# Kernel tuning notes

Measured on AMD Instinct MI355X. Metric: run time of the kernel, lower is better.

The kernel has to match this reference:

```python
import jax, jax.numpy as jnp
import numpy as np

B, N, DIM = 4, 4096, 1024
HEADS, DFF, WIN = 16, 4096, 128
EPS = 1e-5


def _layernorm(x, w, b):
    mu = jnp.mean(x, axis=-1, keepdims=True)
    var = jnp.mean(jnp.square(x - mu), axis=-1, keepdims=True)
    return (x - mu) * jax.lax.rsqrt(var + EPS) * w + b


def _local_attention(q, k, v, window):
    # q,k,v: (B, h, N, d); non-causal, look_backward=1, look_forward=1
    Bq, h, n, d = q.shape
    nb = n // window
    scale = d ** -0.5
    q = q.reshape(Bq * h, nb, window, d) * scale
    k = k.reshape(Bq * h, nb, window, d)
    v = v.reshape(Bq * h, nb, window, d)

    def look_around(t):  # (BH, nb, w, d) -> (BH, nb, 3w, d)
        tp = jnp.pad(t, ((0, 0), (1, 1), (0, 0), (0, 0)))
        return jnp.concatenate([tp[:, :-2], tp[:, 1:-1], tp[:, 2:]], axis=2)

    kk = look_around(k)
    vv = look_around(v)

    # validity mask for out-of-range look-around buckets
    idx = jnp.arange(n).reshape(nb, window)
    idx_p = jnp.pad(idx, ((1, 1), (0, 0)), constant_values=-1)
    kidx = jnp.concatenate([idx_p[:-2], idx_p[1:-1], idx_p[2:]], axis=1)  # (nb, 3w)
    valid = (kidx >= 0)[None, :, None, :]  # (1, nb, 1, 3w)

    sim = jnp.einsum('bnid,bnjd->bnij', q, kk)  # (BH, nb, w, 3w)
    neg = jnp.finfo(sim.dtype).min
    sim = jnp.where(valid, sim, neg)
    attn = jax.nn.softmax(sim, axis=-1)
    out = jnp.einsum('bnij,bnjd->bnid', attn, vv)
    return out.reshape(Bq, h, n, d)


def setup_inputs() -> dict:
    key = jax.random.key(0)
    ks = jax.random.split(key, 8)
    w = lambda k, shape: jax.random.normal(k, shape, jnp.float32) * 0.02
    return {
        'x': jax.random.normal(ks[0], (B, N, DIM), jnp.float32),
        'ln1_w': jnp.ones((DIM,), jnp.float32), 'ln1_b': jnp.zeros((DIM,), jnp.float32),
        'qkv_w': w(ks[1], (3 * DIM, DIM)), 'qkv_b': jnp.zeros((3 * DIM,), jnp.float32),
        'proj_w': w(ks[2], (DIM, DIM)), 'proj_b': jnp.zeros((DIM,), jnp.float32),
        'ln2_w': jnp.ones((DIM,), jnp.float32), 'ln2_b': jnp.zeros((DIM,), jnp.float32),
        'fc1_w': w(ks[3], (DFF, DIM)), 'fc1_b': jnp.zeros((DFF,), jnp.float32),
        'fc2_w': w(ks[4], (DIM, DFF)), 'fc2_b': jnp.zeros((DIM,), jnp.float32),
    }


def reference(x, ln1_w, ln1_b, qkv_w, qkv_b, proj_w, proj_b, ln2_w, ln2_b, fc1_w, fc1_b, fc2_w, fc2_b):
    Bx, n, C = x.shape
    h = HEADS
    hd = C // h
    x_norm = _layernorm(x, ln1_w, ln1_b)
    qkv = x_norm @ qkv_w.T + qkv_b  # (B, N, 3C)
    qkv = qkv.reshape(Bx, n, 3, h, hd).transpose(2, 0, 3, 1, 4)  # (3, B, h, N, hd)
    q, k, v = qkv[0], qkv[1], qkv[2]
    attn_out = _local_attention(q, k, v, WIN)  # (B, h, N, hd)
    attn_out = attn_out.transpose(0, 2, 1, 3).reshape(Bx, n, C)
    x = x + (attn_out @ proj_w.T + proj_b)
    y = _layernorm(x, ln2_w, ln2_b)
    y = jax.nn.gelu(y @ fc1_w.T + fc1_b, approximate=False)
    x = x + (y @ fc2_w.T + fc2_b)
    return x
```

## Files before the change

### kernel.cpp

```cpp
#include <hip/hip_runtime.h>
#include <math.h>

typedef unsigned short u16;
typedef __attribute__((ext_vector_type(4))) float f32x4;
typedef __attribute__((ext_vector_type(8))) __bf16 bf16x8;
typedef __attribute__((ext_vector_type(8))) u16 u16x8;
typedef __attribute__((ext_vector_type(4))) u16 u16x4;

__device__ __forceinline__ float bf2f(u16 v) {
    unsigned int u = ((unsigned int)v) << 16;
    return __builtin_bit_cast(float, u);
}
__device__ __forceinline__ u16 f2bf(float f) {
    unsigned int x = __builtin_bit_cast(unsigned int, f);
    x += 0x7fffu + ((x >> 16) & 1u);
    return (u16)(x >> 16);
}

__device__ __forceinline__ void load_lds16(const u16* g, u16* l) {
    __builtin_amdgcn_global_load_lds((const __attribute__((address_space(1))) void*)g,
                                     (__attribute__((address_space(3))) void*)l, 16, 0, 0);
}

#define WAIT_VM(N) asm volatile("s_waitcnt vmcnt(" #N ")" ::: "memory")
#define LGKM0_SB() do { asm volatile("s_waitcnt lgkmcnt(0)" ::: "memory"); \
                        __builtin_amdgcn_sched_barrier(0); } while (0)
#define MFMA16(d, x, y) d = __builtin_amdgcn_mfma_f32_16x16x32_bf16(x, y, d, 0, 0, 0)

__global__ __launch_bounds__(256) void cvt_kernel(const float* __restrict__ in,
                                                  u16* __restrict__ out, int n)
{
    const int i = (blockIdx.x * 256 + threadIdx.x) * 4;
    if (i >= n) return;
    const float4 f = *(const float4*)(in + i);
    u16x4 o;
    o[0] = f2bf(f.x); o[1] = f2bf(f.y); o[2] = f2bf(f.z); o[3] = f2bf(f.w);
    *(u16x4*)(out + i) = o;
}

template<int EPI, int RES, bool OF32, int NFR>
__global__ __launch_bounds__(512, 2) void gemm256(
    const u16* __restrict__ A, const u16* __restrict__ W,
    const float* __restrict__ bias,
    const float* __restrict__ resf, const u16* __restrict__ resb,
    void* __restrict__ O0v, u16* __restrict__ O1, u16* __restrict__ O2,
    int M, int N, int K, int lda, int ldw, int mbase)
{
    constexpr int BBASE = 16384;
    constexpr int BUFU  = 16384 + NFR * 4096;
    __shared__ u16 S[2 * BUFU];
    const int tid  = threadIdx.x;
    const int w    = tid >> 6;
    const int l    = tid & 63;
    const int colq = l & 15;
    const int quad = l >> 4;
    const int w3   = w & 3;
    const int wm   = (w >> 2) * 128;
    const int wn   = w3 * (NFR * 16);

    const int nX  = (int)gridDim.x;
    const int nwg = nX * (int)gridDim.y;
    const int did = (int)blockIdx.y * nX + (int)blockIdx.x;
    const int q8  = nwg >> 3;
    const int wg  = (nwg & 7) ? did : ((did & 7) * q8 + (did >> 3));
    const int bm  = wg / nX;
    const int bn  = wg - bm * nX;
    const int m0  = bm * 256, n0 = bn * (NFR * 64);

    const int rw   = l >> 3;
    const int sseg = ((l & 7) ^ rw) * 8;
    const u16* gA[2][2];
    const u16* gB[2][2];
#pragma unroll
    for (int h = 0; h < 2; ++h)
#pragma unroll
        for (int j = 0; j < 2; ++j) {
            const int rr = w * 16 + j * 8 + rw;
            gA[h][j] = A + (size_t)(m0 + h * 128 + rr) * lda + sseg;
            if constexpr (NFR == 4) {
                const int nl = (rr >> 5) * 64 + (h * 2 + ((rr >> 4) & 1)) * 16 + (rr & 15);
                gB[h][j] = W + (size_t)(n0 + nl) * ldw + sseg;
            } else if (h == 0) {
                gB[0][j] = W + (size_t)(n0 + rr) * ldw + sseg;
            }
        }
    const int lw = w * 1024;

    const int c0 = (quad * 8) ^ ((colq & 7) << 3);
    const int c1 = c0 ^ 32;

    f32x4 acc[8][NFR] = {};

#pragma unroll
    for (int h = 0; h < 2; ++h)
#pragma unroll
        for (int j = 0; j < 2; ++j)
            load_lds16(gA[h][j], S + h * 8192 + lw + j * 512);
    load_lds16(gB[0][0], S + BBASE + lw);
    load_lds16(gB[0][1], S + BBASE + lw + 512);
    if constexpr (NFR == 4) {
        load_lds16(gB[1][0], S + BBASE + 8192 + lw);
        load_lds16(gB[1][1], S + BBASE + 8192 + lw + 512);
        WAIT_VM(2);
    } else {
        WAIT_VM(0);
    }
    __builtin_amdgcn_s_barrier();

    const int NT = K >> 6;
    for (int t = 0; t < NT; ++t) {
        u16* Sc = S + (t & 1) * BUFU;
        u16* Sn = S + ((t + 1) & 1) * BUFU;
        const int  kk = (t + 1) << 6;
        const bool pf = (t + 1) < NT;

        if constexpr (NFR == 4) {
            bf16x8 aL[4][2], aH[4][2], bL[2][2], bH[2][2];

#pragma unroll
            for (int m = 0; m < 4; ++m) {
                const int rb = (wm + m * 16 + colq) * 64;
                aL[m][0] = *(const bf16x8*)(Sc + rb + c0);
                aL[m][1] = *(const bf16x8*)(Sc + rb + c1);
            }
#pragma unroll
            for (int n = 0; n < 2; ++n) {
                const int rb = BBASE + (w3 * 32 + n * 16 + colq) * 64;
                bL[n][0] = *(const bf16x8*)(Sc + rb + c0);
                bL[n][1] = *(const bf16x8*)(Sc + rb + c1);
            }
            if (pf) {
#pragma unroll
                for (int h = 0; h < 2; ++h)
#pragma unroll
                    for (int j = 0; j < 2; ++j)
                        load_lds16(gA[h][j] + kk, Sn + h * 8192 + lw + j * 512);
            }
            __builtin_amdgcn_s_barrier();
            LGKM0_SB();
            __builtin_amdgcn_s_setprio(1);
#pragma unroll
            for (int m = 0; m < 4; ++m)
#pragma unroll
                for (int n = 0; n < 2; ++n) {
                    MFMA16(acc[m][n], aL[m][0], bL[n][0]);
                    MFMA16(acc[m][n], aL[m][1], bL[n][1]);
                }
            __builtin_amdgcn_s_setprio(0);
            if (pf) { WAIT_VM(4); } else { WAIT_VM(0); }
            __builtin_amdgcn_s_barrier();

#pragma unroll
            for (int n = 0; n < 2; ++n) {
                const int rb = BBASE + 8192 + (w3 * 32 + n * 16 + colq) * 64;
                bH[n][0] = *(const bf16x8*)(Sc + rb + c0);
                bH[n][1] = *(const bf16x8*)(Sc + rb + c1);
            }
            if (pf) {
                load_lds16(gB[0][0] + kk, Sn + BBASE + lw);
                load_lds16(gB[0][1] + kk, Sn + BBASE + lw + 512);
            }
            __builtin_amdgcn_s_barrier();
            LGKM0_SB();
            __builtin_amdgcn_s_setprio(1);
#pragma unroll
            for (int m = 0; m < 4; ++m)
#pragma unroll
                for (int n = 0; n < 2; ++n) {
                    MFMA16(acc[m][2 + n], aL[m][0], bH[n][0]);
                    MFMA16(acc[m][2 + n], aL[m][1], bH[n][1]);
                }
            __builtin_amdgcn_s_setprio(0);
            __builtin_amdgcn_s_barrier();

#pragma unroll
            for (int m = 0; m < 4; ++m) {
                const int rb = (wm + 64 + m * 16 + colq) * 64;
                aH[m][0] = *(const bf16x8*)(Sc + rb + c0);
                aH[m][1] = *(const bf16x8*)(Sc + rb + c1);
            }
            if (pf) {
                load_lds16(gB[1][0] + kk, Sn + BBASE + 8192 + lw);
                load_lds16(gB[1][1] + kk, Sn + BBASE + 8192 + lw + 512);
            }
            __builtin_amdgcn_s_barrier();
            LGKM0_SB();
            __builtin_amdgcn_s_setprio(1);
#pragma unroll
            for (int m = 0; m < 4; ++m)
#pragma unroll
                for (int n = 0; n < 2; ++n) {
                    MFMA16(acc[4 + m][n], aH[m][0], bL[n][0]);
                    MFMA16(acc[4 + m][n], aH[m][1], bL[n][1]);
                }
            __builtin_amdgcn_s_setprio(0);
            __builtin_amdgcn_s_barrier();

            __builtin_amdgcn_s_setprio(1);
#pragma unroll
            for (int m = 0; m < 4; ++m)
#pragma unroll
                for (int n = 0; n < 2; ++n) {
                    MFMA16(acc[4 + m][2 + n], aH[m][0], bH[n][0]);
                    MFMA16(acc[4 + m][2 + n], aH[m][1], bH[n][1]);
                }
            __builtin_amdgcn_s_setprio(0);
            if (pf) { WAIT_VM(2); }
            __builtin_amdgcn_s_barrier();
        } else {
            bf16x8 aL[4][2], aH[4][2], bb[2][2];

#pragma unroll
            for (int m = 0; m < 4; ++m) {
                const int rb = (wm + m * 16 + colq) * 64;
                aL[m][0] = *(const bf16x8*)(Sc + rb + c0);
                aL[m][1] = *(const bf16x8*)(Sc + rb + c1);
            }
#pragma unroll
            for (int n = 0; n < 2; ++n) {
                const int rb = BBASE + (w3 * 32 + n * 16 + colq) * 64;
                bb[n][0] = *(const bf16x8*)(Sc + rb + c0);
                bb[n][1] = *(const bf16x8*)(Sc + rb + c1);
            }
            if (pf) {
#pragma unroll
                for (int h = 0; h < 2; ++h)
#pragma unroll
                    for (int j = 0; j < 2; ++j)
                        load_lds16(gA[h][j] + kk, Sn + h * 8192 + lw + j * 512);
            }
            __builtin_amdgcn_s_barrier();
            LGKM0_SB();
            __builtin_amdgcn_s_setprio(1);
#pragma unroll
            for (int m = 0; m < 4; ++m)
#pragma unroll
                for (int n = 0; n < 2; ++n) {
                    MFMA16(acc[m][n], aL[m][0], bb[n][0]);
                    MFMA16(acc[m][n], aL[m][1], bb[n][1]);
                }
            __builtin_amdgcn_s_setprio(0);
            __builtin_amdgcn_s_barrier();

#pragma unroll
            for (int m = 0; m < 4; ++m) {
                const int rb = (wm + 64 + m * 16 + colq) * 64;
                aH[m][0] = *(const bf16x8*)(Sc + rb + c0);
                aH[m][1] = *(const bf16x8*)(Sc + rb + c1);
            }
            if (pf) {
                load_lds16(gB[0][0] + kk, Sn + BBASE + lw);
                load_lds16(gB[0][1] + kk, Sn + BBASE + lw + 512);
            }
            __builtin_amdgcn_s_barrier();
            LGKM0_SB();
            __builtin_amdgcn_s_setprio(1);
#pragma unroll
            for (int m = 0; m < 4; ++m)
#pragma unroll
                for (int n = 0; n < 2; ++n) {
                    MFMA16(acc[4 + m][n], aH[m][0], bb[n][0]);
                    MFMA16(acc[4 + m][n], aH[m][1], bb[n][1]);
                }
            __builtin_amdgcn_s_setprio(0);
            WAIT_VM(0);
            __builtin_amdgcn_s_barrier();
        }
    }

    if constexpr (EPI == 0) {
        if (n0 >= 2048) {
            __syncthreads();
#pragma unroll
            for (int nf = 0; nf < NFR; ++nf) {
                const int cl = wn + nf * 16 + colq;
                const float bz = bias[n0 + cl];
                const int swz = (cl & 7) << 3;
#pragma unroll
                for (int mf = 0; mf < 8; ++mf) {
                    const int rb = wm + mf * 16 + quad * 4;
                    u16x4 pk;
#pragma unroll
                    for (int i = 0; i < 4; ++i) pk[i] = f2bf(acc[mf][nf][i] + bz);
                    *(u16x4*)(S + cl * 256 + (rb ^ swz)) = pk;
                }
            }
            __syncthreads();
            const int cl   = tid >> 1;
            const int c    = n0 + cl;
            const int head = (c >> 6) & 15;
            const int d    = c & 63;
            const int rg0  = mbase + m0;
            const int bh   = (rg0 >> 12) * 16 + head;
            const int half = tid & 1;
            const int swz  = (cl & 7) << 3;
            u16* op = O2 + ((size_t)bh * 64 + d) * 4096 + (rg0 & 4095) + half * 128;
#pragma unroll
            for (int j = 0; j < 16; ++j) {
                const int r0 = half * 128 + j * 8;
                *(u16x8*)(op + j * 8) = *(const u16x8*)(S + cl * 256 + (r0 ^ swz));
            }
            return;
        }
    }
#pragma unroll
    for (int nf = 0; nf < NFR; ++nf) {
        const int c = n0 + wn + nf * 16 + colq;
        const float bz = bias ? bias[c] : 0.f;
#pragma unroll
        for (int mf = 0; mf < 8; ++mf) {
#pragma unroll
            for (int i = 0; i < 4; ++i) {
                const int r = m0 + wm + mf * 16 + quad * 4 + i;
                float v = acc[mf][nf][i] + bz;
                if constexpr (EPI == 0) {
                    const int head = (c >> 6) & 15;
                    const int d    = c & 63;
                    const int rg   = mbase + r;
                    const int tt   = rg & 4095;
                    const int bh   = (rg >> 12) * 16 + head;
                    const u16 val = f2bf(v);
                    if (c < 1024) ((u16*)O0v)[((size_t)bh * 4096 + tt) * 64 + d] = val;
                    else          O1[((size_t)bh * 4096 + tt) * 64 + d] = val;
                } else {
                    const size_t idx = (size_t)r * N + c;
                    if constexpr (RES == 1) v += resf[idx];
                    if constexpr (RES == 2) v += bf2f(resb[idx]);
                    if constexpr (EPI == 2) v = 0.5f * v * (1.0f + erff(v * 0.70710678118654752f));
                    if constexpr (OF32) ((float*)O0v)[idx] = v;
                    else                ((u16*)O0v)[idx] = f2bf(v);
                }
            }
        }
    }
}

template<bool F32IN>
__global__ __launch_bounds__(256) void ln_kernel(
    const void* __restrict__ xin, const float* __restrict__ w,
    const float* __restrict__ b, u16* __restrict__ out)
{
    const int wave = threadIdx.x >> 6, lane = threadIdx.x & 63;
    const size_t row = (size_t)blockIdx.x * 4 + wave;
    float v[16];
    if constexpr (F32IN) {
        const float* xr = (const float*)xin + row * 1024 + lane * 16;
#pragma unroll
        for (int j = 0; j < 4; ++j) {
            const float4 f = *(const float4*)(xr + j * 4);
            v[j * 4 + 0] = f.x; v[j * 4 + 1] = f.y; v[j * 4 + 2] = f.z; v[j * 4 + 3] = f.w;
        }
    } else {
        const u16* xr = (const u16*)xin + row * 1024 + lane * 16;
        u16x8 xa = *(const u16x8*)xr;
        u16x8 xb = *(const u16x8*)(xr + 8);
#pragma unroll
        for (int i = 0; i < 8; ++i) { v[i] = bf2f(xa[i]); v[8 + i] = bf2f(xb[i]); }
    }
    float s = 0.f, s2 = 0.f;
#pragma unroll
    for (int i = 0; i < 16; ++i) { s += v[i]; s2 += v[i] * v[i]; }
#pragma unroll
    for (int m = 32; m >= 1; m >>= 1) { s += __shfl_xor(s, m, 64); s2 += __shfl_xor(s2, m, 64); }
    const float mu  = s * (1.0f / 1024.0f);
    const float var = s2 * (1.0f / 1024.0f) - mu * mu;
    const float rs  = rsqrtf(var + 1e-5f);
    const float* wp = w + lane * 16;
    const float* bp = b + lane * 16;
    u16x8 oa, ob;
#pragma unroll
    for (int i = 0; i < 8; ++i) {
        oa[i] = f2bf((v[i]     - mu) * rs * wp[i]     + bp[i]);
        ob[i] = f2bf((v[8 + i] - mu) * rs * wp[8 + i] + bp[8 + i]);
    }
    u16* orow = out + row * 1024 + lane * 16;
    *(u16x8*)orow       = oa;
    *(u16x8*)(orow + 8) = ob;
}

__global__ __launch_bounds__(256, 6) void attn_kernel(
    const u16* __restrict__ Q, const u16* __restrict__ Kb,
    const u16* __restrict__ Vt, u16* __restrict__ out)
{
    __shared__ u16 Ps[4][16 * 200];
    const int tid  = threadIdx.x;
    const int wave = tid >> 6;
    const int lane = tid & 63;
    const int colq = lane & 15;
    const int quad = lane >> 4;

    const int f   = blockIdx.x;
    const int xcd = f & 7;
    const int s8  = f >> 3;
    const int bh  = s8 >> 3;
    const int tb  = (s8 & 7) + 8 * xcd;
    const int qrow0 = tb * 64 + wave * 16;
    const int nb    = tb >> 1;
    const int key0  = nb * 128 - 128;
    const int nt_lo = (nb == 0) ? 8 : 0;
    const int nt_hi = (nb == 31) ? 16 : 24;

    const u16* qp = Q + ((size_t)bh * 4096 + qrow0 + colq) * 64 + quad * 8;
    bf16x8 aq0 = *(const bf16x8*)qp;
    bf16x8 aq1 = *(const bf16x8*)(qp + 32);

    float m_i[4], l_i[4];
    f32x4 o[4] = {};
#pragma unroll
    for (int i = 0; i < 4; ++i) { m_i[i] = -3.0e38f; l_i[i] = 0.f; }

    u16* Psw = &Ps[wave][0];

#pragma unroll
    for (int c = 0; c < 2; ++c) {
        const int lo = (c == 0) ? nt_lo : 12;
        const int hi = (c == 0) ? ((nt_hi < 12) ? nt_hi : 12) : nt_hi;

        f32x4 sc[12];
#pragma unroll
        for (int j = 0; j < 12; ++j) {
            const int kr  = key0 + (c * 12 + j) * 16;
            const int krc = kr < 0 ? 0 : (kr > 4080 ? 4080 : kr);
            const u16* kp = Kb + ((size_t)bh * 4096 + krc + colq) * 64 + quad * 8;
            bf16x8 b0 = *(const bf16x8*)kp;
            bf16x8 b1 = *(const bf16x8*)(kp + 32);
            f32x4 z = {0.f, 0.f, 0.f, 0.f};
            z = __builtin_amdgcn_mfma_f32_16x16x32_bf16(aq0, b0, z, 0, 0, 0);
            z = __builtin_amdgcn_mfma_f32_16x16x32_bf16(aq1, b1, z, 0, 0, 0);
            sc[j] = z;
        }
#pragma unroll
        for (int j = 0; j < 12; ++j) {
            const int nt = c * 12 + j;
            if (nt < lo || nt >= hi) {
#pragma unroll
                for (int i = 0; i < 4; ++i) sc[j][i] = -3.0e38f;
            }
        }
        float mc[4];
#pragma unroll
        for (int i = 0; i < 4; ++i) mc[i] = -3.0e38f;
#pragma unroll
        for (int j = 0; j < 12; ++j)
#pragma unroll
            for (int i = 0; i < 4; ++i) mc[i] = fmaxf(mc[i], sc[j][i]);
#pragma unroll
        for (int i = 0; i < 4; ++i)
#pragma unroll
            for (int m = 8; m >= 1; m >>= 1) mc[i] = fmaxf(mc[i], __shfl_xor(mc[i], m, 64));
        float a_i[4], psum[4];
#pragma unroll
        for (int i = 0; i < 4; ++i) {
            const float mn = fmaxf(m_i[i], mc[i]);
            a_i[i] = __expf((m_i[i] - mn) * 0.125f);
            m_i[i] = mn;
            psum[i] = 0.f;
        }
#pragma unroll
        for (int j = 0; j < 12; ++j)
#pragma unroll
            for (int i = 0; i < 4; ++i) {
                const float p = __expf((sc[j][i] - m_i[i]) * 0.125f);
                psum[i] += p;
                Psw[(quad * 4 + i) * 200 + j * 16 + colq] = f2bf(p);
            }
#pragma unroll
        for (int i = 0; i < 4; ++i)
#pragma unroll
            for (int m = 8; m >= 1; m >>= 1) psum[i] += __shfl_xor(psum[i], m, 64);
#pragma unroll
        for (int i = 0; i < 4; ++i) l_i[i] = l_i[i] * a_i[i] + psum[i];
#pragma unroll
        for (int dt = 0; dt < 4; ++dt)
#pragma unroll
            for (int i = 0; i < 4; ++i) o[dt][i] *= a_i[i];
#pragma unroll
        for (int k6 = 0; k6 < 6; ++k6) {
            bf16x8 ap = *(const bf16x8*)(Psw + colq * 200 + k6 * 32 + quad * 8);
            const int kk  = key0 + (c * 6 + k6) * 32 + quad * 8;
            const int kkc = kk < 0 ? 0 : (kk > 4088 ? 4088 : kk);
#pragma unroll
            for (int dt = 0; dt < 4; ++dt) {
                const u16* vp = Vt + ((size_t)bh * 64 + dt * 16 + colq) * 4096 + kkc;
                bf16x8 bv = *(const bf16x8*)vp;
                o[dt] = __builtin_amdgcn_mfma_f32_16x16x32_bf16(ap, bv, o[dt], 0, 0, 0);
            }
        }
    }

    const int bb = bh >> 4, hh = bh & 15;
#pragma unroll
    for (int i = 0; i < 4; ++i) {
        const float inv = 1.0f / fmaxf(l_i[i], 1e-20f);
        const int t = qrow0 + quad * 4 + i;
        u16* op = out + ((size_t)(bb * 4096 + t)) * 1024 + hh * 64;
#pragma unroll
        for (int dt = 0; dt < 4; ++dt) op[dt * 16 + colq] = f2bf(o[dt][i] * inv);
    }
}

extern "C" void kernel_launch(void* const* d_in, const int* in_sizes, int n_in,
                              void* d_out, int out_size, void* d_ws, size_t ws_size,
                              hipStream_t stream)
{
    const float* x      = (const float*)d_in[0];
    const float* ln1_w  = (const float*)d_in[1];
    const float* ln1_b  = (const float*)d_in[2];
    const float* qkv_w  = (const float*)d_in[3];
    const float* qkv_b  = (const float*)d_in[4];
    const float* proj_w = (const float*)d_in[5];
    const float* proj_b = (const float*)d_in[6];
    const float* ln2_w  = (const float*)d_in[7];
    const float* ln2_b  = (const float*)d_in[8];
    const float* fc1_w  = (const float*)d_in[9];
    const float* fc1_b  = (const float*)d_in[10];
    const float* fc2_w  = (const float*)d_in[11];
    const float* fc2_b  = (const float*)d_in[12];
    float* outp = (float*)d_out;

    if (ws_size < 134217728u) return;
    char* ws = (char*)d_ws;
    u16* R0 = (u16*)(ws);
    u16* R1 = (u16*)(ws + 33554432);
    u16* R2 = (u16*)(ws + 67108864);
    u16* R3 = (u16*)(ws + 100663296);
    u16* xnc    = (u16*)d_out;
    u16* attn_o = (u16*)((char*)d_out + 33554432);

    u16* qkvwb  = R0;
    u16* projwb = R0 + 3145728;
    u16* fc1wb  = R0 + 4194304;
    u16* fc2wb  = R0 + 8388608;
    u16* Qb = R1, *Kb = R2, *Vtb = R3;
    u16* x2 = R1;
    u16* yn = attn_o;
    u16* hb = R2;

    cvt_kernel<<<3072, 256, 0, stream>>>(qkv_w, qkvwb, 3145728);
    cvt_kernel<<<1024, 256, 0, stream>>>(proj_w, projwb, 1048576);
    cvt_kernel<<<4096, 256, 0, stream>>>(fc1_w, fc1wb, 4194304);
    cvt_kernel<<<4096, 256, 0, stream>>>(fc2_w, fc2wb, 4194304);
    ln_kernel<true><<<4096, 256, 0, stream>>>(x, ln1_w, ln1_b, xnc);
    gemm256<0, 0, false, 4><<<dim3(12, 64), 512, 0, stream>>>(
        xnc, qkvwb, qkv_b, nullptr, nullptr, Qb, Kb, Vtb,
        16384, 3072, 1024, 1024, 1024, 0);
    attn_kernel<<<4096, 256, 0, stream>>>(Qb, Kb, Vtb, attn_o);
    gemm256<1, 1, false, 4><<<dim3(4, 64), 512, 0, stream>>>(
        attn_o, projwb, proj_b, x, nullptr, x2, nullptr, nullptr,
        16384, 1024, 1024, 1024, 1024, 0);
    ln_kernel<false><<<4096, 256, 0, stream>>>(x2, ln2_w, ln2_b, yn);
    for (int ci = 0; ci < 2; ++ci) {
        const size_t off = (size_t)ci * 8192 * 1024;
        gemm256<2, 0, false, 4><<<dim3(16, 32), 512, 0, stream>>>(
            yn + off, fc1wb, fc1_b, nullptr, nullptr, hb, nullptr, nullptr,
            8192, 4096, 1024, 1024, 1024, 0);
        gemm256<1, 2, true, 2><<<dim3(8, 32), 512, 0, stream>>>(
            hb, fc2wb, fc2_b, nullptr, x2 + off, outp + off, nullptr, nullptr,
            8192, 1024, 4096, 4096, 4096, 0);
    }
}
```

Measured before the change: 1.114 ms.

## Collapse GEMM k-loop to one barrier per tile and skip masked attention tiles

After: 953.1 us. -14.4%, faster.

```diff
diff --git a/kernel.cpp b/kernel.cpp
--- a/kernel.cpp
+++ b/kernel.cpp
@@ -23,9 +23,10 @@
 }
 
 #define WAIT_VM(N) asm volatile("s_waitcnt vmcnt(" #N ")" ::: "memory")
-#define LGKM0_SB() do { asm volatile("s_waitcnt lgkmcnt(0)" ::: "memory"); \
-                        __builtin_amdgcn_sched_barrier(0); } while (0)
 #define MFMA16(d, x, y) d = __builtin_amdgcn_mfma_f32_16x16x32_bf16(x, y, d, 0, 0, 0)
+#define BAR() do { __builtin_amdgcn_sched_barrier(0); asm volatile("" ::: "memory"); \
+                   __builtin_amdgcn_s_barrier();      asm volatile("" ::: "memory"); \
+                   __builtin_amdgcn_sched_barrier(0); } while (0)
 
 __global__ __launch_bounds__(256) void cvt_kernel(const float* __restrict__ in,
                                                   u16* __restrict__ out, int n)
@@ -101,11 +102,9 @@
     if constexpr (NFR == 4) {
         load_lds16(gB[1][0], S + BBASE + 8192 + lw);
         load_lds16(gB[1][1], S + BBASE + 8192 + lw + 512);
-        WAIT_VM(2);
-    } else {
-        WAIT_VM(0);
-    }
-    __builtin_amdgcn_s_barrier();
+    }
+    WAIT_VM(0);
+    BAR();
 
     const int NT = K >> 6;
     for (int t = 0; t < NT; ++t) {
@@ -116,7 +115,6 @@
 
         if constexpr (NFR == 4) {
             bf16x8 aL[4][2], aH[4][2], bL[2][2], bH[2][2];
-
 #pragma unroll
             for (int m = 0; m < 4; ++m) {
                 const int rb = (wm + m * 16 + colq) * 64;
@@ -129,50 +127,12 @@
                 bL[n][0] = *(const bf16x8*)(Sc + rb + c0);
                 bL[n][1] = *(const bf16x8*)(Sc + rb + c1);
             }
-            if (pf) {
-#pragma unroll
-                for (int h = 0; h < 2; ++h)
-#pragma unroll
-                    for (int j = 0; j < 2; ++j)
-                        load_lds16(gA[h][j] + kk, Sn + h * 8192 + lw + j * 512);
-            }
-            __builtin_amdgcn_s_barrier();
-            LGKM0_SB();
-            __builtin_amdgcn_s_setprio(1);
-#pragma unroll
-            for (int m = 0; m < 4; ++m)
-#pragma unroll
-                for (int n = 0; n < 2; ++n) {
-                    MFMA16(acc[m][n], aL[m][0], bL[n][0]);
-                    MFMA16(acc[m][n], aL[m][1], bL[n][1]);
-                }
-            __builtin_amdgcn_s_setprio(0);
-            if (pf) { WAIT_VM(4); } else { WAIT_VM(0); }
-            __builtin_amdgcn_s_barrier();
-
 #pragma unroll
             for (int n = 0; n < 2; ++n) {
                 const int rb = BBASE + 8192 + (w3 * 32 + n * 16 + colq) * 64;
                 bH[n][0] = *(const bf16x8*)(Sc + rb + c0);
                 bH[n][1] = *(const bf16x8*)(Sc + rb + c1);
             }
-            if (pf) {
-                load_lds16(gB[0][0] + kk, Sn + BBASE + lw);
-                load_lds16(gB[0][1] + kk, Sn + BBASE + lw + 512);
-            }
-            __builtin_amdgcn_s_barrier();
-            LGKM0_SB();
-            __builtin_amdgcn_s_setprio(1);
-#pragma unroll
-            for (int m = 0; m < 4; ++m)
-#pragma unroll
-                for (int n = 0; n < 2; ++n) {
-                    MFMA16(acc[m][2 + n], aL[m][0], bH[n][0]);
-                    MFMA16(acc[m][2 + n], aL[m][1], bH[n][1]);
-                }
-            __builtin_amdgcn_s_setprio(0);
-            __builtin_amdgcn_s_barrier();
-
 #pragma unroll
             for (int m = 0; m < 4; ++m) {
                 const int rb = (wm + 64 + m * 16 + colq) * 64;
@@ -180,12 +140,32 @@
                 aH[m][1] = *(const bf16x8*)(Sc + rb + c1);
             }
             if (pf) {
+#pragma unroll
+                for (int h = 0; h < 2; ++h)
+#pragma unroll
+                    for (int j = 0; j < 2; ++j)
+                        load_lds16(gA[h][j] + kk, Sn + h * 8192 + lw + j * 512);
+                load_lds16(gB[0][0] + kk, Sn + BBASE + lw);
+                load_lds16(gB[0][1] + kk, Sn + BBASE + lw + 512);
                 load_lds16(gB[1][0] + kk, Sn + BBASE + 8192 + lw);
                 load_lds16(gB[1][1] + kk, Sn + BBASE + 8192 + lw + 512);
             }
-            __builtin_amdgcn_s_barrier();
-            LGKM0_SB();
+            __builtin_amdgcn_sched_barrier(0);
             __builtin_amdgcn_s_setprio(1);
+#pragma unroll
+            for (int m = 0; m < 4; ++m)
+#pragma unroll
+                for (int n = 0; n < 2; ++n) {
+                    MFMA16(acc[m][n], aL[m][0], bL[n][0]);
+                    MFMA16(acc[m][n], aL[m][1], bL[n][1]);
+                }
+#pragma unroll
+            for (int m = 0; m < 4; ++m)
+#pragma unroll
+                for (int n = 0; n < 2; ++n) {
+                    MFMA16(acc[m][2 + n], aL[m][0], bH[n][0]);
+                    MFMA16(acc[m][2 + n], aL[m][1], bH[n][1]);
+                }
 #pragma unroll
             for (int m = 0; m < 4; ++m)
 #pragma unroll
@@ -193,10 +173,6 @@
                     MFMA16(acc[4 + m][n], aH[m][0], bL[n][0]);
                     MFMA16(acc[4 + m][n], aH[m][1], bL[n][1]);
                 }
-            __builtin_amdgcn_s_setprio(0);
-            __builtin_amdgcn_s_barrier();
-
-            __builtin_amdgcn_s_setprio(1);
 #pragma unroll
             for (int m = 0; m < 4; ++m)
 #pragma unroll
@@ -205,11 +181,8 @@
                     MFMA16(acc[4 + m][2 + n], aH[m][1], bH[n][1]);
                 }
             __builtin_amdgcn_s_setprio(0);
-            if (pf) { WAIT_VM(2); }
-            __builtin_amdgcn_s_barrier();
         } else {
             bf16x8 aL[4][2], aH[4][2], bb[2][2];
-
 #pragma unroll
             for (int m = 0; m < 4; ++m) {
                 const int rb = (wm + m * 16 + colq) * 64;
@@ -222,26 +195,6 @@
                 bb[n][0] = *(const bf16x8*)(Sc + rb + c0);
                 bb[n][1] = *(const bf16x8*)(Sc + rb + c1);
             }
-            if (pf) {
-#pragma unroll
-                for (int h = 0; h < 2; ++h)
-#pragma unroll
-                    for (int j = 0; j < 2; ++j)
-                        load_lds16(gA[h][j] + kk, Sn + h * 8192 + lw + j * 512);
-            }
-            __builtin_amdgcn_s_barrier();
-            LGKM0_SB();
-            __builtin_amdgcn_s_setprio(1);
-#pragma unroll
-            for (int m = 0; m < 4; ++m)
-#pragma unroll
-                for (int n = 0; n < 2; ++n) {
-                    MFMA16(acc[m][n], aL[m][0], bb[n][0]);
-                    MFMA16(acc[m][n], aL[m][1], bb[n][1]);
-                }
-            __builtin_amdgcn_s_setprio(0);
-            __builtin_amdgcn_s_barrier();
-
 #pragma unroll
             for (int m = 0; m < 4; ++m) {
                 const int rb = (wm + 64 + m * 16 + colq) * 64;
@@ -249,12 +202,23 @@
                 aH[m][1] = *(const bf16x8*)(Sc + rb + c1);
             }
             if (pf) {
+#pragma unroll
+                for (int h = 0; h < 2; ++h)
+#pragma unroll
+                    for (int j = 0; j < 2; ++j)
+                        load_lds16(gA[h][j] + kk, Sn + h * 8192 + lw + j * 512);
                 load_lds16(gB[0][0] + kk, Sn + BBASE + lw);
                 load_lds16(gB[0][1] + kk, Sn + BBASE + lw + 512);
             }
-            __builtin_amdgcn_s_barrier();
-            LGKM0_SB();
+            __builtin_amdgcn_sched_barrier(0);
             __builtin_amdgcn_s_setprio(1);
+#pragma unroll
+            for (int m = 0; m < 4; ++m)
+#pragma unroll
+                for (int n = 0; n < 2; ++n) {
+                    MFMA16(acc[m][n], aL[m][0], bb[n][0]);
+                    MFMA16(acc[m][n], aL[m][1], bb[n][1]);
+                }
 #pragma unroll
             for (int m = 0; m < 4; ++m)
 #pragma unroll
@@ -263,9 +227,9 @@
                     MFMA16(acc[4 + m][n], aH[m][1], bb[n][1]);
                 }
             __builtin_amdgcn_s_setprio(0);
-            WAIT_VM(0);
-            __builtin_amdgcn_s_barrier();
-        }
+        }
+        if (pf) { WAIT_VM(0); }
+        BAR();
     }
 
     if constexpr (EPI == 0) {
@@ -378,7 +342,7 @@
     *(u16x8*)(orow + 8) = ob;
 }
 
-__global__ __launch_bounds__(256, 6) void attn_kernel(
+__global__ __launch_bounds__(256, 4) void attn_kernel(
     const u16* __restrict__ Q, const u16* __restrict__ Kb,
     const u16* __restrict__ Vt, u16* __restrict__ out)
 {
@@ -388,6 +352,7 @@
     const int lane = tid & 63;
     const int colq = lane & 15;
     const int quad = lane >> 4;
+    const float C2 = 0.18033688011112042f;
 
     const int f   = blockIdx.x;
     const int xcd = f & 7;
@@ -418,32 +383,32 @@
 
         f32x4 sc[12];
 #pragma unroll
-        for (int j = 0; j < 12; ++j) {
-            const int kr  = key0 + (c * 12 + j) * 16;
-            const int krc = kr < 0 ? 0 : (kr > 4080 ? 4080 : kr);
-            const u16* kp = Kb + ((size_t)bh * 4096 + krc + colq) * 64 + quad * 8;
-            bf16x8 b0 = *(const bf16x8*)kp;
-            bf16x8 b1 = *(const bf16x8*)(kp + 32);
-            f32x4 z = {0.f, 0.f, 0.f, 0.f};
-            z = __builtin_amdgcn_mfma_f32_16x16x32_bf16(aq0, b0, z, 0, 0, 0);
-            z = __builtin_amdgcn_mfma_f32_16x16x32_bf16(aq1, b1, z, 0, 0, 0);
-            sc[j] = z;
-        }
+        for (int j = 0; j < 12; ++j) sc[j] = (f32x4){0.f, 0.f, 0.f, 0.f};
 #pragma unroll
         for (int j = 0; j < 12; ++j) {
             const int nt = c * 12 + j;
-            if (nt < lo || nt >= hi) {
-#pragma unroll
-                for (int i = 0; i < 4; ++i) sc[j][i] = -3.0e38f;
+            if (nt >= lo && nt < hi) {
+                const u16* kp = Kb + ((size_t)bh * 4096 + key0 + nt * 16 + colq) * 64 + quad * 8;
+                bf16x8 b0 = *(const bf16x8*)kp;
+                bf16x8 b1 = *(const bf16x8*)(kp + 32);
+                f32x4 z = {0.f, 0.f, 0.f, 0.f};
+                __builtin_amdgcn_s_setprio(1);
+                z = __builtin_amdgcn_mfma_f32_16x16x32_bf16(aq0, b0, z, 0, 0, 0);
+                z = __builtin_amdgcn_mfma_f32_16x16x32_bf16(aq1, b1, z, 0, 0, 0);
+                __builtin_amdgcn_s_setprio(0);
+                sc[j] = z;
             }
         }
         float mc[4];
 #pragma unroll
         for (int i = 0; i < 4; ++i) mc[i] = -3.0e38f;
 #pragma unroll
-        for (int j = 0; j < 12; ++j)
-#pragma unroll
-            for (int i = 0; i < 4; ++i) mc[i] = fmaxf(mc[i], sc[j][i]);
+        for (int j = 0; j < 12; ++j) {
+            const int nt = c * 12 + j;
+            if (nt >= lo && nt < hi)
+#pragma unroll
+                for (int i = 0; i < 4; ++i) mc[i] = fmaxf(mc[i], sc[j][i]);
+        }
 #pragma unroll
         for (int i = 0; i < 4; ++i)
 #pragma unroll
@@ -452,18 +417,22 @@
 #pragma unroll
         for (int i = 0; i < 4; ++i) {
             const float mn = fmaxf(m_i[i], mc[i]);
-            a_i[i] = __expf((m_i[i] - mn) * 0.125f);
+            a_i[i] = exp2f((m_i[i] - mn) * C2);
             m_i[i] = mn;
             psum[i] = 0.f;
         }
 #pragma unroll
-        for (int j = 0; j < 12; ++j)
-#pragma unroll
-            for (int i = 0; i < 4; ++i) {
-                const float p = __expf((sc[j][i] - m_i[i]) * 0.125f);
-                psum[i] += p;
-                Psw[(quad * 4 + i) * 200 + j * 16 + colq] = f2bf(p);
-            }
+        for (int j = 0; j < 12; ++j) {
+            const int nt = c * 12 + j;
+            if (nt >= lo && nt < hi) {
+#pragma unroll
+                for (int i = 0; i < 4; ++i) {
+                    const float p = exp2f((sc[j][i] - m_i[i]) * C2);
+                    psum[i] += p;
+                    Psw[(quad * 4 + i) * 200 + j * 16 + colq] = f2bf(p);
+                }
+            }
+        }
 #pragma unroll
         for (int i = 0; i < 4; ++i)
 #pragma unroll
@@ -474,16 +443,21 @@
         for (int dt = 0; dt < 4; ++dt)
 #pragma unroll
             for (int i = 0; i < 4; ++i) o[dt][i] *= a_i[i];
+        const int klo = (lo - c * 12) >> 1;
+        const int khi = (hi - c * 12) >> 1;
 #pragma unroll
         for (int k6 = 0; k6 < 6; ++k6) {
-            bf16x8 ap = *(const bf16x8*)(Psw + colq * 200 + k6 * 32 + quad * 8);
-            const int kk  = key0 + (c * 6 + k6) * 32 + quad * 8;
-            const int kkc = kk < 0 ? 0 : (kk > 4088 ? 4088 : kk);
-#pragma unroll
-            for (int dt = 0; dt < 4; ++dt) {
-                const u16* vp = Vt + ((size_t)bh * 64 + dt * 16 + colq) * 4096 + kkc;
-                bf16x8 bv = *(const bf16x8*)vp;
-                o[dt] = __builtin_amdgcn_mfma_f32_16x16x32_bf16(ap, bv, o[dt], 0, 0, 0);
+            if (k6 >= klo && k6 < khi) {
+                bf16x8 ap = *(const bf16x8*)(Psw + colq * 200 + k6 * 32 + quad * 8);
+                const int kkk = key0 + (c * 6 + k6) * 32 + quad * 8;
+                __builtin_amdgcn_s_setprio(1);
+#pragma unroll
+                for (int dt = 0; dt < 4; ++dt) {
+                    const u16* vp = Vt + ((size_t)bh * 64 + dt * 16 + colq) * 4096 + kkk;
+                    bf16x8 bv = *(const bf16x8*)vp;
+                    o[dt] = __builtin_amdgcn_mfma_f32_16x16x32_bf16(ap, bv, o[dt], 0, 0, 0);
+                }
+                __builtin_amdgcn_s_setprio(0);
             }
         }
     }
```
